# Kernel tuning notes

Measured on AMD Instinct MI355X. Metric: run time of the kernel, lower is better.

Reference implementation:

```python
import jax, jax.numpy as jnp
import numpy as np

# ---- static config ----
B, N, C, HF, WF = 2, 256, 256, 64, 64
PATCH = 512
ROI = 15
MARGIN = (ROI - 1) // 2
HID = 256
HEADS = 8
DEPTH = 3
FFN = 1024
NQ = 16
LN_EPS = 1e-5


def setup_inputs() -> dict:
    key = jax.random.key(0)
    ks = jax.random.split(key, 16)
    p = lambda i, shape: (0.02 * jax.random.normal(ks[i], shape, jnp.float32))
    inp = {
        "image_embeddings": jax.random.normal(ks[0], (B, C, HF, WF), jnp.float32),
        "keypoints": jax.random.uniform(ks[1], (B, N, 2), jnp.float32, 0.0, float(PATCH)),
        "keypoints_valid_mask": jax.random.randint(ks[2], (B, N), 0, 2) == 1,
        "proj_w": p(3, (HID, C)), "proj_b": jnp.zeros((HID,), jnp.float32),
        "query_embed": p(4, (NQ, HID)),
        "self_qkv_w": p(5, (DEPTH, 3 * HID, HID)), "self_qkv_b": jnp.zeros((DEPTH, 3 * HID), jnp.float32),
        "self_out_w": p(6, (DEPTH, HID, HID)), "self_out_b": jnp.zeros((DEPTH, HID), jnp.float32),
        "cross_qkv_w": p(7, (DEPTH, 3 * HID, HID)), "cross_qkv_b": jnp.zeros((DEPTH, 3 * HID), jnp.float32),
        "cross_out_w": p(8, (DEPTH, HID, HID)), "cross_out_b": jnp.zeros((DEPTH, HID), jnp.float32),
        "ffn1_w": p(9, (DEPTH, FFN, HID)), "ffn1_b": jnp.zeros((DEPTH, FFN), jnp.float32),
        "ffn2_w": p(10, (DEPTH, HID, FFN)), "ffn2_b": jnp.zeros((DEPTH, HID), jnp.float32),
        "ln1_w": jnp.ones((DEPTH, HID), jnp.float32), "ln1_b": jnp.zeros((DEPTH, HID), jnp.float32),
        "ln2_w": jnp.ones((DEPTH, HID), jnp.float32), "ln2_b": jnp.zeros((DEPTH, HID), jnp.float32),
        "ln3_w": jnp.ones((DEPTH, HID), jnp.float32), "ln3_b": jnp.zeros((DEPTH, HID), jnp.float32),
        "out_w": p(11, (4, HID)), "out_b": jnp.zeros((4,), jnp.float32),
    }
    return inp


def _layer_norm(x, w, b):
    mu = x.mean(-1, keepdims=True)
    var = ((x - mu) ** 2).mean(-1, keepdims=True)
    return (x - mu) * jax.lax.rsqrt(var + LN_EPS) * w + b


def _mha(q_in, kv_in, Wqkv, bqkv, Wo, bo, pad=None):
    # PyTorch nn.MultiheadAttention math (batch_first). pad: [B, S_kv] True=masked.
    Dh = HID // HEADS
    Wq, Wk, Wv = jnp.split(Wqkv, 3, axis=0)
    bq, bk, bv = jnp.split(bqkv, 3, axis=0)
    Bsz = q_in.shape[0]
    q = (q_in @ Wq.T + bq).reshape(Bsz, -1, HEADS, Dh)
    k = (kv_in @ Wk.T + bk).reshape(Bsz, -1, HEADS, Dh)
    v = (kv_in @ Wv.T + bv).reshape(Bsz, -1, HEADS, Dh)
    s = jnp.einsum('bqhd,bkhd->bhqk', q, k) * (Dh ** -0.5)
    if pad is not None:
        s = jnp.where(pad[:, None, None, :], -jnp.inf, s)
    a = jax.nn.softmax(s, axis=-1)
    o = jnp.einsum('bhqk,bkhd->bqhd', a, v).reshape(Bsz, -1, HID)
    return o @ Wo.T + bo


def _roi_sample(img, keypoints):
    # _get_valid_grid + F.grid_sample(bilinear, align_corners=False, zeros padding)
    rc = jnp.round(keypoints)                               # [B,N,2] (r,c), round-half-even like Python round
    off = jnp.arange(-MARGIN, MARGIN + 1, dtype=img.dtype)  # [ROI]
    gy = rc[:, :, 0][..., None, None] + off[:, None]        # [B,N,ROI,ROI] rows
    gx = rc[:, :, 1][..., None, None] + off[None, :]        # [B,N,ROI,ROI] cols
    gxn = gx / (PATCH - 1) * 2.0 - 1.0
    gyn = gy / (PATCH - 1) * 2.0 - 1.0
    invalid = (gxn < -1) | (gyn < -1) | (gxn > 1) | (gyn > 1)  # [B,N,ROI,ROI]
    gxn = jnp.where(invalid, 0.0, gxn)
    gyn = jnp.where(invalid, 0.0, gyn)
    # unnormalize onto the feature map (align_corners=False)
    x = ((gxn + 1.0) * WF - 1.0) * 0.5
    y = ((gyn + 1.0) * HF - 1.0) * 0.5
    x = x.reshape(B, -1)  # [B, P], P = N*ROI*ROI
    y = y.reshape(B, -1)
    x0f = jnp.floor(x); y0f = jnp.floor(y)
    wx = x - x0f; wy = y - y0f
    x0 = x0f.astype(jnp.int32); y0 = y0f.astype(jnp.int32)
    bidx = jnp.arange(B)[:, None]

    def tap(yi, xi, w):
        ok = (yi >= 0) & (yi < HF) & (xi >= 0) & (xi < WF)
        yc = jnp.clip(yi, 0, HF - 1)
        xc = jnp.clip(xi, 0, WF - 1)
        v = img[bidx, :, yc, xc]                 # [B,P,C] gather
        return v * (w * ok)[..., None]

    out = (tap(y0, x0, (1 - wy) * (1 - wx)) + tap(y0, x0 + 1, (1 - wy) * wx)
           + tap(y0 + 1, x0, wy * (1 - wx)) + tap(y0 + 1, x0 + 1, wy * wx))
    feat = out.reshape(B, N, ROI * ROI, C)
    feat = jnp.where(invalid.reshape(B, N, ROI * ROI)[..., None], 0.0, feat)
    return feat  # [B, N, HW, C]


def reference(image_embeddings, keypoints, keypoints_valid_mask, proj_w, proj_b,
              query_embed, self_qkv_w, self_qkv_b, self_out_w, self_out_b,
              cross_qkv_w, cross_qkv_b, cross_out_w, cross_out_b,
              ffn1_w, ffn1_b, ffn2_w, ffn2_b,
              ln1_w, ln1_b, ln2_w, ln2_b, ln3_w, ln3_b, out_w, out_b):
    feat = _roi_sample(image_embeddings, keypoints)                 # [B,N,HW,C]
    mem = jnp.einsum('bnpc,oc->bnpo', feat, proj_w) + proj_b        # 1x1 conv proj
    mem = mem.reshape(B * N, ROI * ROI, HID)
    pad = jnp.broadcast_to(~keypoints_valid_mask.reshape(-1, 1), (B * N, ROI * ROI))
    pad = pad.at[:, 0].set(False)                                    # token 0 always attendable
    tgt = jnp.broadcast_to(query_embed[None], (B * N, NQ, HID))
    for l in range(DEPTH):  # post-norm TransformerDecoderLayer, relu, eval (no dropout)
        sa = _mha(tgt, tgt, self_qkv_w[l], self_qkv_b[l], self_out_w[l], self_out_b[l])
        tgt = _layer_norm(tgt + sa, ln1_w[l], ln1_b[l])
        ca = _mha(tgt, mem, cross_qkv_w[l], cross_qkv_b[l], cross_out_w[l], cross_out_b[l], pad)
        tgt = _layer_norm(tgt + ca, ln2_w[l], ln2_b[l])
        ff = jax.nn.relu(tgt @ ffn1_w[l].T + ffn1_b[l]) @ ffn2_w[l].T + ffn2_b[l]
        tgt = _layer_norm(tgt + ff, ln3_w[l], ln3_b[l])
    out = tgt @ out_w.T + out_b                                      # [B*N, NQ, 4]
    return out.reshape(B, N, NQ, 4)
```

## Files before the change

kernel.cpp:

```cpp
#include <hip/hip_runtime.h>
#include <hip/hip_fp16.h>

#define LB __launch_bounds__(256)

typedef unsigned short u16;
typedef unsigned int   u32;
typedef __attribute__((ext_vector_type(8))) short bf16x8;
typedef __attribute__((ext_vector_type(4))) float f32x4;
typedef __attribute__((ext_vector_type(8))) u16  u16x8;

__device__ __forceinline__ u16 f2b(float f) {
    u32 u = __float_as_uint(f);
    u32 r = (u + 0x7fffu + ((u >> 16) & 1u)) >> 16;
    return (u16)r;
}
__device__ __forceinline__ float b2f(u16 h) {
    return __uint_as_float((u32)h << 16);
}

#define QSCALE 0.17677669529663687f


__global__ void k_prep(const unsigned char* __restrict__ m, int* __restrict__ valid,
                       const float* __restrict__ pb,
                       const float* __restrict__ cqkv_w,
                       const float* __restrict__ cqkv_b,
                       float* __restrict__ ckv)
{
    if (blockIdx.x == 0) {
        __shared__ int flag;
        if (threadIdx.x == 0) flag = 0;
        __syncthreads();
        int loc = 0;
        for (int off = threadIdx.x; off < 512; off += 256)
            if ((off & 3) != 0 && m[off] != 0) loc = 1;
        if (loc) atomicOr(&flag, 1);
        __syncthreads();
        const bool bytelay = (flag != 0);
        for (int s = threadIdx.x; s < 512; s += 256)
            valid[s] = bytelay ? (int)(m[s] != 0) : (int)(((const int*)m)[s] != 0);
    } else {
        const int l = blockIdx.x - 1;
        const float* Wk = cqkv_w + (size_t)l * 196608 + 65536;
        const float* Wv = cqkv_w + (size_t)l * 196608 + 131072;
        const float* kb = cqkv_b + (size_t)l * 768 + 256;
        const float* vb = cqkv_b + (size_t)l * 768 + 512;
        const int o = threadIdx.x;
        float a = 0.f, c = 0.f;
        for (int cc = 0; cc < 256; cc += 4) {
            const float4 p4 = *(const float4*)(pb + cc);
            const float4 k4 = *(const float4*)(Wk + (size_t)o * 256 + cc);
            const float4 v4 = *(const float4*)(Wv + (size_t)o * 256 + cc);
            a += p4.x * k4.x + p4.y * k4.y + p4.z * k4.z + p4.w * k4.w;
            c += p4.x * v4.x + p4.y * v4.y + p4.z * v4.z + p4.w * v4.w;
        }
        ckv[l * 512 + o]       = a + kb[o];
        ckv[l * 512 + 256 + o] = c + vb[o];
    }
}

__global__ LB void k_wconv(const float* __restrict__ s0, const float* __restrict__ s1,
                           const float* __restrict__ s2, const float* __restrict__ s3,
                           const float* __restrict__ s4, const float* __restrict__ s5,
                           const float* __restrict__ s6, u16* __restrict__ dst)
{
    const int e = blockIdx.x * 256 + threadIdx.x;
    if (e >= 3604480) return;
    float v;
    int i = e;
    if (i < 65536) v = s0[i];
    else if ((i -= 65536) < 589824) v = s1[i];
    else if ((i -= 589824) < 196608) v = s2[i];
    else if ((i -= 196608) < 589824) v = s3[i];
    else if ((i -= 589824) < 196608) v = s4[i];
    else if ((i -= 196608) < 786432) v = s5[i];
    else if ((i -= 786432) < 786432) v = s6[i];
    else {
        i -= 786432;
        const int l = i / 131072;
        const int r = (i - l * 131072) >> 8;
        const int c = i & 255;
        v = s3[(size_t)l * 196608 + (size_t)(256 + r) * 256 + c];
    }
    dst[e] = f2b(v);
}

__global__ LB void k_transpose(const float* __restrict__ img, u16* __restrict__ imgTb)
{
    __shared__ float tile[64][65];
    const int b  = blockIdx.z;
    const int c0 = blockIdx.y * 64;
    const int p0 = blockIdx.x * 64;
    const int t  = threadIdx.x;
    const int tr = t >> 6, tc = t & 63;
#pragma unroll
    for (int p = 0; p < 16; ++p) {
        const int i = p * 4 + tr;
        tile[i][tc] = img[((size_t)(b * 256 + c0 + i)) * 4096 + p0 + tc];
    }
    __syncthreads();
#pragma unroll
    for (int p = 0; p < 16; ++p) {
        const int jj = p * 4 + tr;
        imgTb[((size_t)(b * 4096 + p0 + jj)) * 256 + c0 + tc] = f2b(tile[tc][jj]);
    }
}

template<int BM>
__global__ LB void gemm_mfma(const u16* __restrict__ A, const u16* __restrict__ W,
                             const float* __restrict__ bias,
                             float* __restrict__ Cf, u16* __restrict__ Cb,
                             int M, int N, int K, int relu)
{
    constexpr int BN = 128;
    __shared__ u16 lds[2][(BM + BN) * 64];
    const int t = threadIdx.x;
    const int wid = t >> 6, lane = t & 63;
    const int bm = blockIdx.y * BM, bn = blockIdx.x * BN;
    const int KT = K >> 6;

    auto stage = [&](int buf, int kt) {
        const int k0 = kt * 64;
        const int rr = t >> 3;
        const int u  = t & 7;
#pragma unroll
        for (int q = 0; q < BM / 32; ++q) {
            const int r = q * 32 + rr;
            const u16* src = A + (size_t)(bm + r) * K + k0 + ((u ^ (r & 7)) << 3);
            __builtin_amdgcn_global_load_lds(
                (const __attribute__((address_space(1))) void*)src,
                (__attribute__((address_space(3))) void*)&lds[buf][q * 2048 + wid * 512],
                16, 0, 0);
        }
#pragma unroll
        for (int q = 0; q < 4; ++q) {
            const int r = q * 32 + rr;
            const u16* src = W + (size_t)(bn + r) * K + k0 + ((u ^ (r & 7)) << 3);
            __builtin_amdgcn_global_load_lds(
                (const __attribute__((address_space(1))) void*)src,
                (__attribute__((address_space(3))) void*)&lds[buf][BM * 64 + q * 2048 + wid * 512],
                16, 0, 0);
        }
    };

    const int wr = wid >> 1, wc = wid & 1;
    constexpr int MR = BM / 32;
    f32x4 acc[MR][4];
    const f32x4 z = {0.f, 0.f, 0.f, 0.f};
#pragma unroll
    for (int mi = 0; mi < MR; ++mi)
#pragma unroll
        for (int ni = 0; ni < 4; ++ni) acc[mi][ni] = z;

    const int r16 = lane & 15, kg = lane >> 4;

    stage(0, 0);
    int cur = 0;
    for (int kt = 0; kt < KT; ++kt) {
        asm volatile("s_waitcnt vmcnt(0)" ::: "memory");
        __syncthreads();
        if (kt + 1 < KT) stage(cur ^ 1, kt + 1);
        const u16* pA = lds[cur];
        const u16* pB = lds[cur] + BM * 64;
#pragma unroll
        for (int kk = 0; kk < 2; ++kk) {
            const int s = kk * 4 + kg;
            bf16x8 afr[MR], bfr[4];
#pragma unroll
            for (int mi = 0; mi < MR; ++mi) {
                const int r = wr * (BM / 2) + mi * 16 + r16;
                afr[mi] = *(const bf16x8*)(pA + r * 64 + ((s ^ (r & 7)) << 3));
            }
#pragma unroll
            for (int ni = 0; ni < 4; ++ni) {
                const int c = wc * 64 + ni * 16 + r16;
                bfr[ni] = *(const bf16x8*)(pB + c * 64 + ((s ^ (c & 7)) << 3));
            }
#pragma unroll
            for (int mi = 0; mi < MR; ++mi)
#pragma unroll
                for (int ni = 0; ni < 4; ++ni)
                    acc[mi][ni] = __builtin_amdgcn_mfma_f32_16x16x32_bf16(
                        afr[mi], bfr[ni], acc[mi][ni], 0, 0, 0);
        }
        cur ^= 1;
    }

#pragma unroll
    for (int mi = 0; mi < MR; ++mi) {
#pragma unroll
        for (int ni = 0; ni < 4; ++ni) {
            const int col = bn + wc * 64 + ni * 16 + r16;
            const float bs = bias ? bias[col] : 0.0f;
#pragma unroll
            for (int rg = 0; rg < 4; ++rg) {
                const int row = bm + wr * (BM / 2) + mi * 16 + kg * 4 + rg;
                float v = acc[mi][ni][rg] + bs;
                if (relu) v = fmaxf(v, 0.0f);
                if (Cf) Cf[(size_t)row * N + col] = v;
                if (Cb) Cb[(size_t)row * N + col] = f2b(v);
            }
        }
    }
}

__global__ LB void gemm_ln(const u16* __restrict__ A, const u16* __restrict__ W,
                           const float* __restrict__ bias,
                           float* __restrict__ tgt, u16* __restrict__ tgtb,
                           const float* __restrict__ lnw, const float* __restrict__ lnb,
                           int K)
{
    __shared__ u16 lA[32 * 64];
    __shared__ u16 lB[256 * 64];
    __shared__ float psum[2][32];
    __shared__ float psq[2][32];
    const int t = threadIdx.x;
    const int wid = t >> 6, lane = t & 63;
    const int r16 = lane & 15, kg = lane >> 4;
    const int wr = wid >> 1, wc = wid & 1;
    const int bm = blockIdx.x * 32;
    const int KT = K >> 6;

    f32x4 acc[8];
    const f32x4 z = {0.f, 0.f, 0.f, 0.f};
#pragma unroll
    for (int ni = 0; ni < 8; ++ni) acc[ni] = z;

    for (int kt = 0; kt < KT; ++kt) {
        const int k0 = kt * 64;
        const int rr = t >> 3;
        const int u  = t & 7;
        {
            const int r = rr;
            const u16* src = A + (size_t)(bm + r) * K + k0 + ((u ^ (r & 7)) << 3);
            __builtin_amdgcn_global_load_lds(
                (const __attribute__((address_space(1))) void*)src,
                (__attribute__((address_space(3))) void*)&lA[wid * 512],
                16, 0, 0);
        }
#pragma unroll
        for (int q = 0; q < 8; ++q) {
            const int r = q * 32 + rr;
            const u16* src = W + (size_t)r * K + k0 + ((u ^ (r & 7)) << 3);
            __builtin_amdgcn_global_load_lds(
                (const __attribute__((address_space(1))) void*)src,
                (__attribute__((address_space(3))) void*)&lB[q * 2048 + wid * 512],
                16, 0, 0);
        }
        asm volatile("s_waitcnt vmcnt(0)" ::: "memory");
        __syncthreads();
#pragma unroll
        for (int kk = 0; kk < 2; ++kk) {
            const int s = kk * 4 + kg;
            const int ra = wr * 16 + r16;
            const bf16x8 afr = *(const bf16x8*)(lA + ra * 64 + ((s ^ (ra & 7)) << 3));
#pragma unroll
            for (int ni = 0; ni < 8; ++ni) {
                const int c = wc * 128 + ni * 16 + r16;
                const bf16x8 bfr = *(const bf16x8*)(lB + c * 64 + ((s ^ (c & 7)) << 3));
                acc[ni] = __builtin_amdgcn_mfma_f32_16x16x32_bf16(afr, bfr, acc[ni], 0, 0, 0);
            }
        }
        __syncthreads();
    }

    float xv[4][8];
    float bcol[8], wcol[8], bncol[8];
#pragma unroll
    for (int ni = 0; ni < 8; ++ni) {
        const int c = wc * 128 + ni * 16 + r16;
        bcol[ni]  = bias[c];
        wcol[ni]  = lnw[c];
        bncol[ni] = lnb[c];
    }
#pragma unroll
    for (int rg = 0; rg < 4; ++rg) {
        const int row = bm + wr * 16 + kg * 4 + rg;
#pragma unroll
        for (int ni = 0; ni < 8; ++ni) {
            const int c = wc * 128 + ni * 16 + r16;
            xv[rg][ni] = tgt[(size_t)row * 256 + c] + acc[ni][rg] + bcol[ni];
        }
    }
#pragma unroll
    for (int rg = 0; rg < 4; ++rg) {
        float s = 0.f;
#pragma unroll
        for (int ni = 0; ni < 8; ++ni) s += xv[rg][ni];
#pragma unroll
        for (int m = 1; m < 16; m <<= 1) s += __shfl_xor(s, m);
        if (r16 == 0) psum[wc][wr * 16 + kg * 4 + rg] = s;
    }
    __syncthreads();
    float mu[4];
#pragma unroll
    for (int rg = 0; rg < 4; ++rg) {
        const int rl = wr * 16 + kg * 4 + rg;
        mu[rg] = (psum[0][rl] + psum[1][rl]) * (1.0f / 256.0f);
    }
#pragma unroll
    for (int rg = 0; rg < 4; ++rg) {
        float q = 0.f;
#pragma unroll
        for (int ni = 0; ni < 8; ++ni) {
            const float d = xv[rg][ni] - mu[rg];
            q += d * d;
        }
#pragma unroll
        for (int m = 1; m < 16; m <<= 1) q += __shfl_xor(q, m);
        if (r16 == 0) psq[wc][wr * 16 + kg * 4 + rg] = q;
    }
    __syncthreads();
#pragma unroll
    for (int rg = 0; rg < 4; ++rg) {
        const int rl = wr * 16 + kg * 4 + rg;
        const int row = bm + rl;
        const float var = (psq[0][rl] + psq[1][rl]) * (1.0f / 256.0f);
        const float inv = 1.0f / sqrtf(var + 1e-5f);
#pragma unroll
        for (int ni = 0; ni < 8; ++ni) {
            const int c = wc * 128 + ni * 16 + r16;
            const float o = (xv[rg][ni] - mu[rg]) * inv * wcol[ni] + bncol[ni];
            tgt[(size_t)row * 256 + c]  = o;
            tgtb[(size_t)row * 256 + c] = f2b(o);
        }
    }
}

__global__ LB void k_init_tgt(float* __restrict__ tgt, u16* __restrict__ tgtb,
                              const float* __restrict__ qe)
{
    const int e = blockIdx.x * 256 + threadIdx.x;
    const int c = e & 255;
    const int row = e >> 8;
    const int i = row & 15;
    const float v = qe[(i << 8) | c];
    tgt[e] = v;
    tgtb[e] = f2b(v);
}

__global__ LB void k_self_attn(const u16* __restrict__ QKV, u16* __restrict__ O)
{
    const int blk = blockIdx.x;
    const int s = blk >> 3, h = blk & 7;
    __shared__ float q_s[16][36], k_s[16][36], v_s[16][36];
    __shared__ float e_s[16][17];
    __shared__ float rsum[16];
    const int t = threadIdx.x;
    const int i = t >> 4, j = t & 15;

    const u16* basep = QKV + (size_t)(s * 16 + i) * 768 + h * 32;
    q_s[i][j]      = b2f(basep[j]);
    q_s[i][j + 16] = b2f(basep[j + 16]);
    k_s[i][j]      = b2f(basep[256 + j]);
    k_s[i][j + 16] = b2f(basep[256 + j + 16]);
    v_s[i][j]      = b2f(basep[512 + j]);
    v_s[i][j + 16] = b2f(basep[512 + j + 16]);
    __syncthreads();

    float acc = 0.0f;
#pragma unroll
    for (int d = 0; d < 32; d += 4) {
        const float4 q4 = *(const float4*)(&q_s[i][d]);
        const float4 k4 = *(const float4*)(&k_s[j][d]);
        acc += q4.x * k4.x + q4.y * k4.y + q4.z * k4.z + q4.w * k4.w;
    }
    const float sc = acc * QSCALE;
    e_s[i][j] = sc;
    __syncthreads();
    float mx = e_s[i][0];
#pragma unroll
    for (int x = 1; x < 16; ++x) mx = fmaxf(mx, e_s[i][x]);
    const float e = __expf(sc - mx);
    __syncthreads();
    e_s[i][j] = e;
    __syncthreads();
    if (j == 0) {
        float sm = 0.0f;
#pragma unroll
        for (int x = 0; x < 16; ++x) sm += e_s[i][x];
        rsum[i] = sm;
    }
    __syncthreads();

    const int oi = t >> 5;
    const int d  = t & 31;
#pragma unroll
    for (int pass = 0; pass < 2; ++pass) {
        const int r = oi + pass * 8;
        float o = 0.0f;
#pragma unroll
        for (int x = 0; x < 16; ++x) o += e_s[r][x] * v_s[x][d];
        O[(size_t)(s * 16 + r) * 256 + h * 32 + d] = f2b(o / rsum[r]);
    }
}

__global__ LB void k_cross_attn(const u16* __restrict__ Qb,
                                const u16* __restrict__ KV, int kvs,
                                const float* __restrict__ ckv,
                                const int* __restrict__ valid,
                                const float* __restrict__ kps,
                                u16* __restrict__ O)
{
    __shared__ __align__(16) char arena[64832];
    u16* Wm  = (u16*)arena;
    u16* WmT = (u16*)(arena + 14400);

    const int t = threadIdx.x;
    const int lane = t & 63, wid = t >> 6;
    const int r16 = lane & 15, kg = lane >> 4;
    const int blk = blockIdx.x;
    const int s = blk >> 1;
    const int h = (blk & 1) * 4 + wid;
    const int b = s >> 8, n = s & 255;

    u16* buf = (u16*)(arena + 22848 + wid * 10496);
    u16* p_b = (u16*)(arena + 22848 + wid * 10496 + 2048);
    u16* QP  = p_b;

    for (int e = t; e < 16208; e += 256) ((u32*)arena)[e] = 0;
    __syncthreads();

    const float kpy = kps[(b * 256 + n) * 2 + 0];
    const float kpx = kps[(b * 256 + n) * 2 + 1];
    const float gx0 = rintf(kpx) - 7.0f;
    const float gy0 = rintf(kpy) - 7.0f;
    const float gxn0 = gx0 / 511.0f * 2.0f - 1.0f;
    const float gyn0 = gy0 / 511.0f * 2.0f - 1.0f;
    const float xb = ((gxn0 + 1.f) * 64.f - 1.f) * 0.5f;
    const float yb = ((gyn0 + 1.f) * 64.f - 1.f) * 0.5f;
    const int x0b = (int)floorf(xb);
    const int y0b = (int)floorf(yb);

    if (t < 225) {
        const int iy = t / 15, ix = t - iy * 15;
        const float gy = rintf(kpy) + (float)(iy - 7);
        const float gx = rintf(kpx) + (float)(ix - 7);
        const float gxn = gx / 511.0f * 2.0f - 1.0f;
        const float gyn = gy / 511.0f * 2.0f - 1.0f;
        const bool inval = (gxn < -1.f) || (gyn < -1.f) || (gxn > 1.f) || (gyn > 1.f);
        const float x = ((gxn + 1.f) * 64.f - 1.f) * 0.5f;
        const float y = ((gyn + 1.f) * 64.f - 1.f) * 0.5f;
        const float x0f = floorf(x), y0f = floorf(y);
        const float wx = x - x0f, wy = y - y0f;
        const int x0 = (int)x0f, y0 = (int)y0f;
#pragma unroll
        for (int tt = 0; tt < 4; ++tt) {
            const int dy = tt >> 1, dx = tt & 1;
            const int yi = y0 + dy, xi = x0 + dx;
            const bool ok = (yi >= 0) && (yi < 64) && (xi >= 0) && (xi < 64) && !inval;
            const float w = (dy ? wy : 1.f - wy) * (dx ? wx : 1.f - wx);
            if (ok) {
                const int cell = (yi - y0b) * 4 + (xi - x0b);
                const u16 wb = f2b(w);
                Wm[t * 32 + ((((cell >> 3) ^ (t & 3)) << 3) | (cell & 7))] = wb;
                WmT[cell * 264 + t] = wb;
            }
        }
    }
    const int cell = lane >> 2, ch8 = (lane & 3) * 8;
    const int cy = cell >> 2, cx = cell & 3;
    const int py = min(max(y0b + cy, 0), 63);
    const int px = min(max(x0b + cx, 0), 63);
    const size_t texidx = (size_t)(b * 4096 + py * 64 + px) * kvs + h * 32 + ch8;
    *(u16x8*)(buf + cell * 32 + ch8) = *(const u16x8*)(KV + texidx);
    const bool vld = valid[s] != 0;
    __syncthreads();


    {
        const bf16x8 qfr = *(const bf16x8*)(Qb + (size_t)(s * 16 + r16) * 256 + h * 32 + kg * 8);
        const bf16x8 tfr = *(const bf16x8*)(buf + r16 * 32 + kg * 8);
        f32x4 aq = {0.f, 0.f, 0.f, 0.f};
        aq = __builtin_amdgcn_mfma_f32_16x16x32_bf16(qfr, tfr, aq, 0, 0, 0);
#pragma unroll
        for (int rg = 0; rg < 4; ++rg)
            QP[(kg * 4 + rg) * 40 + r16] = f2b(aq[rg]);
    }

    float ev[4][15];
    {
        const bf16x8 afr = *(const bf16x8*)(QP + r16 * 40 + kg * 8);
#pragma unroll
        for (int tile = 0; tile < 15; ++tile) {
            const int p = tile * 16 + r16;
            const int rc = p < 225 ? p : 224;
            const bf16x8 bfr = *(const bf16x8*)(Wm + rc * 32 + ((kg ^ (rc & 3)) << 3));
            f32x4 acc = {0.f, 0.f, 0.f, 0.f};
            acc = __builtin_amdgcn_mfma_f32_16x16x32_bf16(afr, bfr, acc, 0, 0, 0);
#pragma unroll
            for (int rg = 0; rg < 4; ++rg) {
                float sv = acc[rg] * QSCALE;
                if (p > 224) sv = -1e30f;
                if (!vld && p > 0) sv = -1e30f;
                ev[rg][tile] = sv;
            }
        }
    }
    float rowsumv[4];
#pragma unroll
    for (int rg = 0; rg < 4; ++rg) {
        float mx = -1e30f;
#pragma unroll
        for (int k = 0; k < 15; ++k) mx = fmaxf(mx, ev[rg][k]);
#pragma unroll
        for (int m = 1; m < 16; m <<= 1) mx = fmaxf(mx, __shfl_xor(mx, m));
        float ps = 0.f;
#pragma unroll
        for (int k = 0; k < 15; ++k) {
            ev[rg][k] = __expf(ev[rg][k] - mx);
            ps += ev[rg][k];
        }
#pragma unroll
        for (int m = 1; m < 16; m <<= 1) ps += __shfl_xor(ps, m);
        rowsumv[rg] = ps;
    }

#pragma unroll
    for (int rg = 0; rg < 4; ++rg)
#pragma unroll
        for (int k = 0; k < 15; ++k) {
            const int p = k * 16 + r16;
            if (p < 225) p_b[(kg * 4 + rg) * 264 + p] = f2b(ev[rg][k]);
        }
    for (int e = lane; e < 496; e += 64) {
        const int row = e / 31;
        p_b[row * 264 + 225 + (e - row * 31)] = 0;
    }

    {
        const u16x8 v = *(const u16x8*)(KV + texidx + 256);
#pragma unroll
        for (int j = 0; j < 8; ++j)
            buf[(ch8 + j) * 32 + cell] = ((const u16*)&v)[j];
        const int zr = lane & 15, zc0 = 16 + (lane >> 4) * 4;
#pragma unroll
        for (int j = 0; j < 4; ++j) buf[zr * 32 + zc0 + j] = 0;
    }

    f32x4 pw = {0.f, 0.f, 0.f, 0.f};
#pragma unroll
    for (int ks = 0; ks < 8; ++ks) {
        const bf16x8 pa = *(const bf16x8*)(p_b + r16 * 264 + ks * 32 + kg * 8);
        const bf16x8 wb = *(const bf16x8*)(WmT + r16 * 264 + ks * 32 + kg * 8);
        pw = __builtin_amdgcn_mfma_f32_16x16x32_bf16(pa, wb, pw, 0, 0, 0);
    }

#pragma unroll
    for (int rg = 0; rg < 4; ++rg)
        QP[(kg * 4 + rg) * 40 + r16] = f2b(pw[rg]);
    {
        const int zq = lane & 15, zc0 = 16 + (lane >> 4) * 4;
#pragma unroll
        for (int j = 0; j < 4; ++j) QP[zq * 40 + zc0 + j] = 0;
    }

#pragma unroll
    for (int ct = 0; ct < 2; ++ct) {
        const bf16x8 pa = *(const bf16x8*)(QP + r16 * 40 + kg * 8);
        const bf16x8 vb = *(const bf16x8*)(buf + (ct * 16 + r16) * 32 + kg * 8);
        f32x4 ao = {0.f, 0.f, 0.f, 0.f};
        ao = __builtin_amdgcn_mfma_f32_16x16x32_bf16(pa, vb, ao, 0, 0, 0);
#pragma unroll
        for (int rg = 0; rg < 4; ++rg) {
            const int q = kg * 4 + rg;
            const int ch = h * 32 + ct * 16 + r16;
            const float val = ao[rg] / rowsumv[rg] + ckv[256 + ch];
            O[(size_t)(s * 16 + q) * 256 + ch] = f2b(val);
        }
    }
}

__global__ LB void k_out(const float* __restrict__ X, const float* __restrict__ W,
                         const float* __restrict__ bias, float* __restrict__ O)
{
    __shared__ float w_s[4][260];
    const int t = threadIdx.x;
    for (int e = t; e < 1024; e += 256) w_s[e >> 8][e & 255] = W[e];
    __syncthreads();
    const int row = blockIdx.x * 64 + (t >> 2);
    const int j = t & 3;
    const float4* xr = (const float4*)(X + (size_t)row * 256);
    float acc = 0.0f;
#pragma unroll
    for (int k4 = 0; k4 < 64; ++k4) {
        const float4 x = xr[k4];
        acc += x.x * w_s[j][k4 * 4]     + x.y * w_s[j][k4 * 4 + 1]
             + x.z * w_s[j][k4 * 4 + 2] + x.w * w_s[j][k4 * 4 + 3];
    }
    O[(size_t)row * 4 + j] = acc + bias[j];
}

extern "C" void kernel_launch(void* const* d_in, const int* in_sizes, int n_in,
                              void* d_out, int out_size, void* d_ws, size_t ws_size,
                              hipStream_t stream)
{
    const float* img          = (const float*)d_in[0];
    const float* kps          = (const float*)d_in[1];
    const unsigned char* vmsk = (const unsigned char*)d_in[2];
    const float* proj_w       = (const float*)d_in[3];
    const float* proj_b       = (const float*)d_in[4];
    const float* query_embed  = (const float*)d_in[5];
    const float* self_qkv_w   = (const float*)d_in[6];
    const float* self_qkv_b   = (const float*)d_in[7];
    const float* self_out_w   = (const float*)d_in[8];
    const float* self_out_b   = (const float*)d_in[9];
    const float* cross_qkv_w  = (const float*)d_in[10];
    const float* cross_qkv_b  = (const float*)d_in[11];
    const float* cross_out_w  = (const float*)d_in[12];
    const float* cross_out_b  = (const float*)d_in[13];
    const float* ffn1_w       = (const float*)d_in[14];
    const float* ffn1_b       = (const float*)d_in[15];
    const float* ffn2_w       = (const float*)d_in[16];
    const float* ffn2_b       = (const float*)d_in[17];
    const float* ln1_w        = (const float*)d_in[18];
    const float* ln1_b        = (const float*)d_in[19];
    const float* ln2_w        = (const float*)d_in[20];
    const float* ln2_b        = (const float*)d_in[21];
    const float* ln3_w        = (const float*)d_in[22];
    const float* ln3_b        = (const float*)d_in[23];
    const float* out_w        = (const float*)d_in[24];
    const float* out_b        = (const float*)d_in[25];
    float* out = (float*)d_out;

    char* W8 = (char*)d_ws;
    size_t off = 0;
    auto alloc = [&](size_t bytes) { void* p = W8 + off; off += (bytes + 255) & ~(size_t)255; return p; };
    float* tgt   = (float*)alloc(2097152 * 4);
    u16* Qb      = (u16*)alloc(2097152 * 2);
    u16* Sb16    = (u16*)alloc(6291456 * 2);
    float* ckv   = (float*)alloc(3 * 512 * 4);
    u16* imgTb   = (u16*)alloc(2097152 * 2);
    u16* imgPb   = (u16*)alloc(2097152 * 2);
    u16* KVb3    = (u16*)alloc(12582912 * 2);
    u16* tgtb    = (u16*)alloc(2097152 * 2);
    u16* Abuf    = (u16*)alloc(2097152 * 2);
    u16* Hbuf    = (u16*)alloc(8388608 * 2);
    u16* wAll    = (u16*)alloc(3604480 * 2);
    int* valid   = (int*)alloc(512 * 4);

    u16* wProj = wAll;
    u16* wSQKV = wProj + 65536;
    u16* wSOut = wSQKV + 589824;
    u16* wCQKV = wSOut + 196608;
    u16* wCOut = wCQKV + 589824;
    u16* wF1   = wCOut + 196608;
    u16* wF2   = wF1 + 786432;
    u16* wCKV3 = wF2 + 786432;

    k_prep<<<4, 256, 0, stream>>>(vmsk, valid, proj_b, cross_qkv_w, cross_qkv_b, ckv);
    k_wconv<<<14080, 256, 0, stream>>>(proj_w, self_qkv_w, self_out_w, cross_qkv_w,
                                       cross_out_w, ffn1_w, ffn2_w, wAll);
    k_transpose<<<dim3(64, 4, 2), 256, 0, stream>>>(img, imgTb);
    gemm_mfma<64><<<dim3(2, 128), 256, 0, stream>>>(imgTb, wProj, nullptr,
                                                    nullptr, imgPb, 8192, 256, 256, 0);
    gemm_mfma<128><<<dim3(12, 64), 256, 0, stream>>>(imgPb, wCKV3, nullptr,
                                                     nullptr, KVb3, 8192, 1536, 256, 0);
    k_init_tgt<<<8192, 256, 0, stream>>>(tgt, tgtb, query_embed);

    for (int l = 0; l < 3; ++l) {
        gemm_mfma<128><<<dim3(6, 64), 256, 0, stream>>>(tgtb, wSQKV + (size_t)l * 196608,
            self_qkv_b + (size_t)l * 768, nullptr, Sb16, 8192, 768, 256, 0);
        k_self_attn<<<4096, 256, 0, stream>>>(Sb16, Abuf);
        gemm_ln<<<256, 256, 0, stream>>>(Abuf, wSOut + (size_t)l * 65536,
            self_out_b + (size_t)l * 256, tgt, tgtb,
            ln1_w + (size_t)l * 256, ln1_b + (size_t)l * 256, 256);

        gemm_mfma<64><<<dim3(2, 128), 256, 0, stream>>>(tgtb, wCQKV + (size_t)l * 196608,
            cross_qkv_b + (size_t)l * 768, nullptr, Qb, 8192, 256, 256, 0);
        k_cross_attn<<<1024, 256, 0, stream>>>(Qb, KVb3 + (size_t)l * 512, 1536,
                                               ckv + (size_t)l * 512, valid, kps, Abuf);
        gemm_ln<<<256, 256, 0, stream>>>(Abuf, wCOut + (size_t)l * 65536,
            cross_out_b + (size_t)l * 256, tgt, tgtb,
            ln2_w + (size_t)l * 256, ln2_b + (size_t)l * 256, 256);

        gemm_mfma<128><<<dim3(8, 64), 256, 0, stream>>>(tgtb, wF1 + (size_t)l * 262144,
            ffn1_b + (size_t)l * 1024, nullptr, Hbuf, 8192, 1024, 256, 1);
        gemm_ln<<<256, 256, 0, stream>>>(Hbuf, wF2 + (size_t)l * 262144,
            ffn2_b + (size_t)l * 256, tgt, tgtb,
            ln3_w + (size_t)l * 256, ln3_b + (size_t)l * 256, 1024);
    }

    k_out<<<128, 256, 0, stream>>>(tgt, out_w, out_b, out);
}
```

Before: 407.1 us.

## Rewrite self-attention with per-wave MFMA and shrink GEMM row tiles

The self-attention kernel now has one wavefront per (sequence, head) pair and computes QK^T and PV with bf16 MFMA instructions. Row max and row sum are done with lane shuffles instead of shared-memory passes and block barriers, and the launch drops from 4096 blocks to 1024. The self-QKV and FFN1 GEMMs also move from 128-row to 64-row tiles, doubling their grid sizes for more parallelism. The attention probabilities are rounded to bf16 before the PV product, so accuracy is slightly lower, and there is no barrier between the per-wave LDS writes and reads, which relies on wavefront-level ordering.

```diff
diff --git a/kernel.cpp b/kernel.cpp
--- a/kernel.cpp
+++ b/kernel.cpp
@@ -341,57 +341,67 @@
 
 __global__ LB void k_self_attn(const u16* __restrict__ QKV, u16* __restrict__ O)
 {
+    __shared__ __align__(16) u16 arena[4][1536];
+    const int t = threadIdx.x;
+    const int lane = t & 63, wid = t >> 6;
+    const int r16 = lane & 15, kg = lane >> 4;
     const int blk = blockIdx.x;
-    const int s = blk >> 3, h = blk & 7;
-    __shared__ float q_s[16][36], k_s[16][36], v_s[16][36];
-    __shared__ float e_s[16][17];
-    __shared__ float rsum[16];
-    const int t = threadIdx.x;
-    const int i = t >> 4, j = t & 15;
-
-    const u16* basep = QKV + (size_t)(s * 16 + i) * 768 + h * 32;
-    q_s[i][j]      = b2f(basep[j]);
-    q_s[i][j + 16] = b2f(basep[j + 16]);
-    k_s[i][j]      = b2f(basep[256 + j]);
-    k_s[i][j + 16] = b2f(basep[256 + j + 16]);
-    v_s[i][j]      = b2f(basep[512 + j]);
-    v_s[i][j + 16] = b2f(basep[512 + j + 16]);
-    __syncthreads();
-
-    float acc = 0.0f;
-#pragma unroll
-    for (int d = 0; d < 32; d += 4) {
-        const float4 q4 = *(const float4*)(&q_s[i][d]);
-        const float4 k4 = *(const float4*)(&k_s[j][d]);
-        acc += q4.x * k4.x + q4.y * k4.y + q4.z * k4.z + q4.w * k4.w;
-    }
-    const float sc = acc * QSCALE;
-    e_s[i][j] = sc;
-    __syncthreads();
-    float mx = e_s[i][0];
-#pragma unroll
-    for (int x = 1; x < 16; ++x) mx = fmaxf(mx, e_s[i][x]);
-    const float e = __expf(sc - mx);
-    __syncthreads();
-    e_s[i][j] = e;
-    __syncthreads();
-    if (j == 0) {
-        float sm = 0.0f;
-#pragma unroll
-        for (int x = 0; x < 16; ++x) sm += e_s[i][x];
-        rsum[i] = sm;
-    }
-    __syncthreads();
-
-    const int oi = t >> 5;
-    const int d  = t & 31;
-#pragma unroll
-    for (int pass = 0; pass < 2; ++pass) {
-        const int r = oi + pass * 8;
-        float o = 0.0f;
-#pragma unroll
-        for (int x = 0; x < 16; ++x) o += e_s[r][x] * v_s[x][d];
-        O[(size_t)(s * 16 + r) * 256 + h * 32 + d] = f2b(o / rsum[r]);
+    const int s = blk >> 1;
+    const int h = (blk & 1) * 4 + wid;
+
+    u16* p_lds = &arena[wid][0];
+    u16* vT    = &arena[wid][512];
+
+    const bf16x8 qfr = *(const bf16x8*)(QKV + (size_t)(s * 16 + r16) * 768 + h * 32 + kg * 8);
+    const bf16x8 kfr = *(const bf16x8*)(QKV + (size_t)(s * 16 + r16) * 768 + 256 + h * 32 + kg * 8);
+    f32x4 sv = {0.f, 0.f, 0.f, 0.f};
+    sv = __builtin_amdgcn_mfma_f32_16x16x32_bf16(qfr, kfr, sv, 0, 0, 0);
+
+    float ev[4], rowsum[4];
+#pragma unroll
+    for (int rg = 0; rg < 4; ++rg) ev[rg] = sv[rg] * QSCALE;
+#pragma unroll
+    for (int rg = 0; rg < 4; ++rg) {
+        float mx = ev[rg];
+#pragma unroll
+        for (int m = 1; m < 16; m <<= 1) mx = fmaxf(mx, __shfl_xor(mx, m));
+        ev[rg] = __expf(ev[rg] - mx);
+        float ps = ev[rg];
+#pragma unroll
+        for (int m = 1; m < 16; m <<= 1) ps += __shfl_xor(ps, m);
+        rowsum[rg] = ps;
+    }
+
+#pragma unroll
+    for (int rg = 0; rg < 4; ++rg)
+        p_lds[(kg * 4 + rg) * 32 + r16] = f2b(ev[rg]);
+    {
+        const int zq = lane & 15, zc = 16 + (lane >> 4) * 4;
+#pragma unroll
+        for (int j = 0; j < 4; ++j) p_lds[zq * 32 + zc + j] = 0;
+    }
+    {
+        const int key = lane >> 2, ch8 = (lane & 3) * 8;
+        const u16x8 v = *(const u16x8*)(QKV + (size_t)(s * 16 + key) * 768 + 512 + h * 32 + ch8);
+#pragma unroll
+        for (int j = 0; j < 8; ++j)
+            vT[(ch8 + j) * 32 + key] = ((const u16*)&v)[j];
+        const int zc0 = lane >> 1, zk0 = 16 + (lane & 1) * 8;
+#pragma unroll
+        for (int j = 0; j < 8; ++j) vT[zc0 * 32 + zk0 + j] = 0;
+    }
+
+#pragma unroll
+    for (int ct = 0; ct < 2; ++ct) {
+        const bf16x8 pa = *(const bf16x8*)(p_lds + r16 * 32 + kg * 8);
+        const bf16x8 vb = *(const bf16x8*)(vT + (ct * 16 + r16) * 32 + kg * 8);
+        f32x4 ao = {0.f, 0.f, 0.f, 0.f};
+        ao = __builtin_amdgcn_mfma_f32_16x16x32_bf16(pa, vb, ao, 0, 0, 0);
+#pragma unroll
+        for (int rg = 0; rg < 4; ++rg) {
+            const int q = kg * 4 + rg;
+            O[(size_t)(s * 16 + q) * 256 + h * 32 + ct * 16 + r16] = f2b(ao[rg] / rowsum[rg]);
+        }
     }
 }
 
@@ -466,7 +476,6 @@
     *(u16x8*)(buf + cell * 32 + ch8) = *(const u16x8*)(KV + texidx);
     const bool vld = valid[s] != 0;
     __syncthreads();
-
 
     {
         const bf16x8 qfr = *(const bf16x8*)(Qb + (size_t)(s * 16 + r16) * 256 + h * 32 + kg * 8);
@@ -659,9 +668,9 @@
     k_init_tgt<<<8192, 256, 0, stream>>>(tgt, tgtb, query_embed);
 
     for (int l = 0; l < 3; ++l) {
-        gemm_mfma<128><<<dim3(6, 64), 256, 0, stream>>>(tgtb, wSQKV + (size_t)l * 196608,
+        gemm_mfma<64><<<dim3(6, 128), 256, 0, stream>>>(tgtb, wSQKV + (size_t)l * 196608,
             self_qkv_b + (size_t)l * 768, nullptr, Sb16, 8192, 768, 256, 0);
-        k_self_attn<<<4096, 256, 0, stream>>>(Sb16, Abuf);
+        k_self_attn<<<1024, 256, 0, stream>>>(Sb16, Abuf);
         gemm_ln<<<256, 256, 0, stream>>>(Abuf, wSOut + (size_t)l * 65536,
             self_out_b + (size_t)l * 256, tgt, tgtb,
             ln1_w + (size_t)l * 256, ln1_b + (size_t)l * 256, 256);
@@ -674,7 +683,7 @@
             cross_out_b + (size_t)l * 256, tgt, tgtb,
             ln2_w + (size_t)l * 256, ln2_b + (size_t)l * 256, 256);
 
-        gemm_mfma<128><<<dim3(8, 64), 256, 0, stream>>>(tgtb, wF1 + (size_t)l * 262144,
+        gemm_mfma<64><<<dim3(8, 128), 256, 0, stream>>>(tgtb, wF1 + (size_t)l * 262144,
             ffn1_b + (size_t)l * 1024, nullptr, Hbuf, 8192, 1024, 256, 1);
         gemm_ln<<<256, 256, 0, stream>>>(Hbuf, wF2 + (size_t)l * 262144,
             ffn2_b + (size_t)l * 256, tgt, tgtb,
```

New measurement: 382.6 us. 1.06x faster.
